# Optimization experiments

Hardware: AMD Instinct MI355X
Metric: run time of the kernel (lower is better)

The kernel has to match this reference:

```python
import jax, jax.numpy as jnp
import numpy as np

NUM_HEADS = 16
FEAT_DIM = 1024
COORD_DIM = 128
D_FEAT = FEAT_DIM // NUM_HEADS   # 64
D_COORD = COORD_DIM // NUM_HEADS # 8

def setup_inputs() -> dict:
    key = jax.random.key(0)
    ks = jax.random.split(key, 5)
    B, L, S = 2, 2048, 2048
    qf = jax.random.normal(ks[0], (B, L, FEAT_DIM), dtype=jnp.float32)
    kf = jax.random.normal(ks[1], (B, S, FEAT_DIM), dtype=jnp.float32)
    qc = jax.random.normal(ks[2], (B, L, COORD_DIM), dtype=jnp.float32)
    kc = jax.random.normal(ks[3], (B, S, COORD_DIM), dtype=jnp.float32)
    v = jax.random.normal(ks[4], (B, S, FEAT_DIM), dtype=jnp.float32)
    alpha = jnp.ones((NUM_HEADS,), dtype=jnp.float32)
    return {"qf": qf, "kf": kf, "qc": qc, "kc": kc, "v": v, "alpha": alpha}

def _split_heads(x):
    # (B, L, H*D) -> (B, H, L, D)
    B, L, HD = x.shape
    return x.reshape(B, L, NUM_HEADS, HD // NUM_HEADS).transpose(0, 2, 1, 3)

def reference(qf, kf, qc, kc, v, alpha):
    qfh = _split_heads(qf)  # (B,H,L,Df)
    kfh = _split_heads(kf)  # (B,H,S,Df)
    qch = _split_heads(qc)  # (B,H,L,Dc)
    kch = _split_heads(kc)  # (B,H,S,Dc)
    vh = _split_heads(v)    # (B,H,S,Dv)
    # A = softmax(Qf Kf^T / sqrt(Df) + alpha * Qc Kc^T / sqrt(Dc))
    inv_sf = 1.0 / np.sqrt(D_FEAT).astype(np.float32)
    inv_sc = 1.0 / np.sqrt(D_COORD).astype(np.float32)
    scores = (jnp.einsum('bhld,bhsd->bhls', qfh, kfh) * inv_sf
              + alpha[None, :, None, None]
              * jnp.einsum('bhld,bhsd->bhls', qch, kch) * inv_sc)
    attn = jax.nn.softmax(scores, axis=-1)
    out = jnp.einsum('bhls,bhsd->bhld', attn, vh)  # (B,H,L,Dv)
    B, H, L, Dv = out.shape
    return out.transpose(0, 2, 1, 3).reshape(B, L, H * Dv)
```

## Files before the change

### kernel.cpp

```cpp
#include <hip/hip_runtime.h>
#include <hip/hip_bf16.h>

typedef __bf16 bf16_t;
typedef bf16_t bf16x8 __attribute__((ext_vector_type(8)));
typedef float f32x4 __attribute__((ext_vector_type(4)));
typedef float f32x16 __attribute__((ext_vector_type(16)));

#define NHEADS 16
#define DFEAT 64
#define DCOORD 8
#define SEQ 2048
#define KVBLK 64
#define NT (SEQ / KVBLK)
#define QBLK 128
#define KCOLS 96
#define KROWB (KCOLS * 2)
#define KTILEB (KVBLK * KROWB)
#define VTILEB (KVBLK * DFEAT * 2)
#define VTILE_ELEMS (KVBLK * DFEAT)

#define KP_BYTES ((size_t)32 * NT * KTILEB)
#define VT_BYTES ((size_t)32 * NT * VTILEB)

union Bf8 { bf16x8 v; __hip_bfloat16 e[8]; };
union U4  { unsigned u[4]; bf16x8 v; };

static __device__ inline unsigned pack2(float a, float b) {
    union { __hip_bfloat16 h[2]; unsigned u; } x;
    x.h[0] = __float2bfloat16(a); x.h[1] = __float2bfloat16(b);
    return x.u;
}

__global__ __launch_bounds__(256)
void pack_k(const float* __restrict__ kf, const float* __restrict__ kc,
            char* __restrict__ kp)
{
    __shared__ __align__(16) char tile[KTILEB];
    const int blk = blockIdx.x;
    const int t  = blk & (NT - 1);
    const int bh = blk >> 5;
    const int b = bh >> 4, h = bh & 15;
    const int tid = threadIdx.x;
    #pragma unroll
    for (int it = 0; it < 2; ++it) {
        const int c = tid + it * 256;
        if (c < 384) {
            const int row = c / 6, cc = c - row * 6;
            const int s = t * KVBLK + row;
            float v[16];
            if (cc < 4) {
                const float* p = kf + ((long)b * SEQ + s) * (NHEADS * DFEAT) + h * DFEAT + cc * 16;
                #pragma unroll
                for (int i = 0; i < 4; ++i) {
                    float4 f = ((const float4*)p)[i];
                    v[4*i+0]=f.x; v[4*i+1]=f.y; v[4*i+2]=f.z; v[4*i+3]=f.w;
                }
            } else if (cc == 4) {
                const float* p = kc + ((long)b * SEQ + s) * (NHEADS * DCOORD) + h * DCOORD;
                float4 f0 = ((const float4*)p)[0];
                float4 f1 = ((const float4*)p)[1];
                v[0]=f0.x; v[1]=f0.y; v[2]=f0.z; v[3]=f0.w;
                v[4]=f1.x; v[5]=f1.y; v[6]=f1.z; v[7]=f1.w;
                #pragma unroll
                for (int i = 8; i < 16; ++i) v[i] = 0.f;
            } else {
                #pragma unroll
                for (int i = 0; i < 16; ++i) v[i] = 0.f;
            }
            Bf8 w0, w1;
            #pragma unroll
            for (int i = 0; i < 8; ++i) {
                w0.e[i] = __float2bfloat16(v[i]);
                w1.e[i] = __float2bfloat16(v[i + 8]);
            }
            const int key  = ((cc < 4) ? (row & 7) : (row & 3)) << 4;
            const int base = cc * 32;
            *(bf16x8*)&tile[row * KROWB + ((base)      ^ key)] = w0.v;
            *(bf16x8*)&tile[row * KROWB + ((base + 16) ^ key)] = w1.v;
        }
    }
    __syncthreads();
    const bf16x8* ti = (const bf16x8*)tile;
    bf16x8* o = (bf16x8*)(kp + (long)blk * KTILEB);
    #pragma unroll
    for (int j = 0; j < 3; ++j) o[tid + 256 * j] = ti[tid + 256 * j];
}

__global__ __launch_bounds__(256)
void pack_v(const float* __restrict__ v, __hip_bfloat16* __restrict__ vt)
{
    __shared__ __align__(16) __hip_bfloat16 tile[VTILE_ELEMS];
    const int blk = blockIdx.x;
    const int t  = blk & (NT - 1);
    const int bh = blk >> 5;
    const int b = bh >> 4, h = bh & 15;
    const int tid = threadIdx.x;
    const int s = tid >> 2, c = tid & 3;
    const int slot = (s & ~12) | ((s & 4) << 1) | ((s & 8) >> 1);
    const float* src = v + ((long)b * SEQ + t * KVBLK + s) * (NHEADS * DFEAT) + h * DFEAT;
    #pragma unroll
    for (int c4 = 0; c4 < 4; ++c4) {
        float4 f = ((const float4*)src)[c4 * 4 + c];
        float vals[4] = {f.x, f.y, f.z, f.w};
        #pragma unroll
        for (int ii = 0; ii < 4; ++ii) {
            const int dd = c4 * 16 + c * 4 + ii;
            const int byte = (dd * 128 + slot * 2) ^ ((dd & 7) << 4);
            tile[byte >> 1] = __float2bfloat16(vals[ii]);
        }
    }
    __syncthreads();
    const bf16x8* ti = (const bf16x8*)tile;
    bf16x8* o = (bf16x8*)(vt + (long)blk * VTILE_ELEMS);
    o[tid]       = ti[tid];
    o[tid + 256] = ti[tid + 256];
}

__global__ __launch_bounds__(256, 2)
void stfa_v5(const float* __restrict__ qf, const float* __restrict__ qc,
             const float* __restrict__ alpha,
             const char* __restrict__ kp, const char* __restrict__ vt,
             float* __restrict__ out)
{
    __shared__ __align__(16) char Kbuf[2][KTILEB];
    __shared__ __align__(16) char Vbuf[2][VTILEB];

    const int tid  = threadIdx.x;
    const int wave = tid >> 6;
    const int lane = tid & 63;
    const int lq   = lane & 31;
    const int hi   = lane >> 5;

    const int dd    = blockIdx.x;
    const int bh    = dd & 31;
    const int qtile = dd >> 5;
    const int b = bh >> 4, h = bh & 15;

    const float a_h      = alpha[h];
    const float LOG2E    = 1.4426950408889634f;
    const float qf_scale = 0.125f * LOG2E;
    const float qc_scale = a_h * 0.35355339059327373f * LOG2E;

    const char* kp_bh = kp + (long)bh * NT * KTILEB;
    const char* vt_bh = (const char*)vt + (long)bh * NT * VTILEB;

    auto stage = [&](int bb, int t) {
        const char* kg = kp_bh + (long)t * KTILEB;
        const char* vg = vt_bh + (long)t * VTILEB;
        char* kl = &Kbuf[bb][0];
        char* vl = &Vbuf[bb][0];
        #pragma unroll
        for (int j = 0; j < 3; ++j) {
            const int i = wave + 4 * j;
            __builtin_amdgcn_global_load_lds(
                (const __attribute__((address_space(1))) void*)(kg + i * 1024 + lane * 16),
                (__attribute__((address_space(3))) void*)(kl + i * 1024), 16, 0, 0);
        }
        #pragma unroll
        for (int j = 0; j < 2; ++j) {
            const int i = wave * 2 + j;
            __builtin_amdgcn_global_load_lds(
                (const __attribute__((address_space(1))) void*)(vg + i * 1024 + lane * 16),
                (__attribute__((address_space(3))) void*)(vl + i * 1024), 16, 0, 0);
        }
    };

    stage(0, 0);

    const int qrow = qtile * QBLK + wave * 32 + lq;
    const float* qfp = qf + ((long)b * SEQ + qrow) * (NHEADS * DFEAT) + h * DFEAT;
    const float* qcp = qc + ((long)b * SEQ + qrow) * (NHEADS * DCOORD) + h * DCOORD;

    bf16x8 qfrag[5];
    #pragma unroll
    for (int ks = 0; ks < 4; ++ks) {
        const float* p = qfp + ks * 16 + hi * 8;
        float4 f0 = *(const float4*)p;
        float4 f1 = *(const float4*)(p + 4);
        Bf8 q;
        q.e[0] = __float2bfloat16(f0.x * qf_scale); q.e[1] = __float2bfloat16(f0.y * qf_scale);
        q.e[2] = __float2bfloat16(f0.z * qf_scale); q.e[3] = __float2bfloat16(f0.w * qf_scale);
        q.e[4] = __float2bfloat16(f1.x * qf_scale); q.e[5] = __float2bfloat16(f1.y * qf_scale);
        q.e[6] = __float2bfloat16(f1.z * qf_scale); q.e[7] = __float2bfloat16(f1.w * qf_scale);
        qfrag[ks] = q.v;
    }
    {
        Bf8 q;
        #pragma unroll
        for (int i = 0; i < 8; ++i) q.e[i] = __float2bfloat16(0.0f);
        if (hi == 0) {
            float4 c0 = *(const float4*)qcp;
            float4 c1 = *(const float4*)(qcp + 4);
            q.e[0] = __float2bfloat16(c0.x * qc_scale); q.e[1] = __float2bfloat16(c0.y * qc_scale);
            q.e[2] = __float2bfloat16(c0.z * qc_scale); q.e[3] = __float2bfloat16(c0.w * qc_scale);
            q.e[4] = __float2bfloat16(c1.x * qc_scale); q.e[5] = __float2bfloat16(c1.y * qc_scale);
            q.e[6] = __float2bfloat16(c1.z * qc_scale); q.e[7] = __float2bfloat16(c1.w * qc_scale);
        }
        qfrag[4] = q.v;
    }

    f32x16 oacc[2];
    #pragma unroll
    for (int dt = 0; dt < 2; ++dt)
        #pragma unroll
        for (int r = 0; r < 16; ++r) oacc[dt][r] = 0.f;
    float l_part = 0.f;

    __syncthreads();

    for (int t = 0; t < NT; ++t) {
        const int bb = t & 1;
        if (t + 1 < NT) stage(bb ^ 1, t + 1);

        f32x16 sacc[2];
        #pragma unroll
        for (int st = 0; st < 2; ++st)
            #pragma unroll
            for (int r = 0; r < 16; ++r) sacc[st][r] = 0.f;
        __builtin_amdgcn_s_setprio(1);
        #pragma unroll
        for (int st = 0; st < 2; ++st) {
            const int row = st * 32 + lq;
            #pragma unroll
            for (int ks = 0; ks < 5; ++ks) {
                const int off = ks * 32 + hi * 16;
                const int key = ((ks < 4) ? (lq & 7) : (lq & 3)) << 4;
                bf16x8 kfrag = *(const bf16x8*)&Kbuf[bb][row * KROWB + (off ^ key)];
                sacc[st] = __builtin_amdgcn_mfma_f32_32x32x16_bf16(kfrag, qfrag[ks], sacc[st], 0, 0, 0);
            }
        }
        __builtin_amdgcn_s_setprio(0);

        bf16x8 pfrag[4];
        float lsum = 0.f;
        #pragma unroll
        for (int T = 0; T < 2; ++T) {
            float p[16];
            #pragma unroll
            for (int r = 0; r < 16; ++r) p[r] = __builtin_amdgcn_exp2f(sacc[T][r]);
            U4 fa, fb;
            #pragma unroll
            for (int i = 0; i < 4; ++i) {
                fa.u[i] = pack2(p[2 * i],     p[2 * i + 1]);
                fb.u[i] = pack2(p[2 * i + 8], p[2 * i + 9]);
            }
            pfrag[2 * T]     = fa.v;
            pfrag[2 * T + 1] = fb.v;
            float s8[8];
            #pragma unroll
            for (int r = 0; r < 8; ++r) s8[r] = p[r] + p[r + 8];
            float s4[4];
            #pragma unroll
            for (int r = 0; r < 4; ++r) s4[r] = s8[r] + s8[r + 4];
            lsum += (s4[0] + s4[1]) + (s4[2] + s4[3]);
        }
        l_part += lsum;

        __builtin_amdgcn_s_setprio(1);
        #pragma unroll
        for (int dt = 0; dt < 2; ++dt) {
            const int row = dt * 32 + lq;
            #pragma unroll
            for (int ks = 0; ks < 4; ++ks) {
                bf16x8 vfrag = *(const bf16x8*)&Vbuf[bb][row * 128 + ((ks * 32 + hi * 16) ^ ((lq & 7) << 4))];
                oacc[dt] = __builtin_amdgcn_mfma_f32_32x32x16_bf16(vfrag, pfrag[ks], oacc[dt], 0, 0, 0);
            }
        }
        __builtin_amdgcn_s_setprio(0);

        __syncthreads();
    }

    const float l = l_part + __shfl_xor(l_part, 32);
    const float invl = 1.0f / l;

    float* ob = out + ((long)b * SEQ + qrow) * (NHEADS * DFEAT) + h * DFEAT;
    #pragma unroll
    for (int dt = 0; dt < 2; ++dt) {
        #pragma unroll
        for (int g = 0; g < 4; ++g) {
            const int d0 = dt * 32 + g * 8 + hi * 4;
            float4 o;
            o.x = oacc[dt][4 * g + 0] * invl;
            o.y = oacc[dt][4 * g + 1] * invl;
            o.z = oacc[dt][4 * g + 2] * invl;
            o.w = oacc[dt][4 * g + 3] * invl;
            *(float4*)(ob + d0) = o;
        }
    }
}

__global__ __launch_bounds__(256)
void stfa_v1(const float* __restrict__ qf, const float* __restrict__ kf,
             const float* __restrict__ qc, const float* __restrict__ kc,
             const float* __restrict__ vv, const float* __restrict__ alpha,
             float* __restrict__ out)
{
    __shared__ __align__(16) __hip_bfloat16 Klds[64 * 104];
    __shared__ __align__(16) __hip_bfloat16 Vlds[64 * 72];
    __shared__ __align__(16) __hip_bfloat16 Plds[4 * 16 * 72];

    const int tid  = threadIdx.x;
    const int wave = tid >> 6;
    const int lane = tid & 63;
    const int lr   = lane & 15;
    const int lg   = lane >> 4;

    const int blk   = blockIdx.x;
    const int qtile = blk & 31;
    const int h     = (blk >> 5) & 15;
    const int b     = blk >> 9;

    for (int i = tid; i < 64 * 104; i += 256) Klds[i] = __float2bfloat16(0.0f);

    const float a_h      = alpha[h];
    const float LOG2E    = 1.4426950408889634f;
    const float qf_scale = 0.125f * LOG2E;
    const float qc_scale = a_h * 0.35355339059327373f * LOG2E;

    const int qrow = qtile * 64 + wave * 16 + lr;
    const float* qf_p = qf + ((long)b * SEQ + qrow) * 1024 + h * 64;
    const float* qc_p = qc + ((long)b * SEQ + qrow) * 128 + h * 8;

    bf16x8 qfrag[3];
    #pragma unroll
    for (int st = 0; st < 2; ++st) {
        const float* p = qf_p + st * 32 + lg * 8;
        float4 f0 = *(const float4*)p;
        float4 f1 = *(const float4*)(p + 4);
        Bf8 q;
        q.e[0] = __float2bfloat16(f0.x * qf_scale); q.e[1] = __float2bfloat16(f0.y * qf_scale);
        q.e[2] = __float2bfloat16(f0.z * qf_scale); q.e[3] = __float2bfloat16(f0.w * qf_scale);
        q.e[4] = __float2bfloat16(f1.x * qf_scale); q.e[5] = __float2bfloat16(f1.y * qf_scale);
        q.e[6] = __float2bfloat16(f1.z * qf_scale); q.e[7] = __float2bfloat16(f1.w * qf_scale);
        qfrag[st] = q.v;
    }
    {
        Bf8 q;
        #pragma unroll
        for (int i = 0; i < 8; ++i) q.e[i] = __float2bfloat16(0.0f);
        if (lg == 0) {
            float4 c0 = *(const float4*)qc_p;
            float4 c1 = *(const float4*)(qc_p + 4);
            q.e[0] = __float2bfloat16(c0.x * qc_scale); q.e[1] = __float2bfloat16(c0.y * qc_scale);
            q.e[2] = __float2bfloat16(c0.z * qc_scale); q.e[3] = __float2bfloat16(c0.w * qc_scale);
            q.e[4] = __float2bfloat16(c1.x * qc_scale); q.e[5] = __float2bfloat16(c1.y * qc_scale);
            q.e[6] = __float2bfloat16(c1.z * qc_scale); q.e[7] = __float2bfloat16(c1.w * qc_scale);
        }
        qfrag[2] = q.v;
    }

    const float* kf_b = kf + (long)b * SEQ * 1024 + h * 64;
    const float* kc_b = kc + (long)b * SEQ * 128 + h * 8;
    const float* v_b  = vv + (long)b * SEQ * 1024 + h * 64;

    f32x4 oacc[4];
    #pragma unroll
    for (int ct = 0; ct < 4; ++ct) { oacc[ct][0]=0.f; oacc[ct][1]=0.f; oacc[ct][2]=0.f; oacc[ct][3]=0.f; }
    float m_r[4], l_r[4];
    #pragma unroll
    for (int j = 0; j < 4; ++j) { m_r[j] = -3.0e38f; l_r[j] = 0.f; }

    __syncthreads();

    for (int s0 = 0; s0 < SEQ; s0 += 64) {
        {
            const int srow = tid >> 2, ch = tid & 3;
            const float* p = kf_b + (long)(s0 + srow) * 1024 + ch * 16;
            float4 f0 = ((const float4*)p)[0];
            float4 f1 = ((const float4*)p)[1];
            float4 f2 = ((const float4*)p)[2];
            float4 f3 = ((const float4*)p)[3];
            Bf8 w0, w1;
            w0.e[0]=__float2bfloat16(f0.x); w0.e[1]=__float2bfloat16(f0.y);
            w0.e[2]=__float2bfloat16(f0.z); w0.e[3]=__float2bfloat16(f0.w);
            w0.e[4]=__float2bfloat16(f1.x); w0.e[5]=__float2bfloat16(f1.y);
            w0.e[6]=__float2bfloat16(f1.z); w0.e[7]=__float2bfloat16(f1.w);
            w1.e[0]=__float2bfloat16(f2.x); w1.e[1]=__float2bfloat16(f2.y);
            w1.e[2]=__float2bfloat16(f2.z); w1.e[3]=__float2bfloat16(f2.w);
            w1.e[4]=__float2bfloat16(f3.x); w1.e[5]=__float2bfloat16(f3.y);
            w1.e[6]=__float2bfloat16(f3.z); w1.e[7]=__float2bfloat16(f3.w);
            *(bf16x8*)&Klds[srow * 104 + ch * 16]     = w0.v;
            *(bf16x8*)&Klds[srow * 104 + ch * 16 + 8] = w1.v;
        }
        {
            const int srow = tid >> 2, cp = (tid & 3) * 2;
            const float* p = kc_b + (long)(s0 + srow) * 128 + cp;
            float2 c = *(const float2*)p;
            Klds[srow * 104 + 64 + cp]     = __float2bfloat16(c.x);
            Klds[srow * 104 + 64 + cp + 1] = __float2bfloat16(c.y);
        }
        {
            const int srow = tid & 63, d0 = (tid >> 6) * 16;
            const float* p = v_b + (long)(s0 + srow) * 1024 + d0;
            #pragma unroll
            for (int c4 = 0; c4 < 4; ++c4) {
                float4 f = ((const float4*)p)[c4];
                Vlds[(d0 + c4 * 4 + 0) * 72 + srow] = __float2bfloat16(f.x);
                Vlds[(d0 + c4 * 4 + 1) * 72 + srow] = __float2bfloat16(f.y);
                Vlds[(d0 + c4 * 4 + 2) * 72 + srow] = __float2bfloat16(f.z);
                Vlds[(d0 + c4 * 4 + 3) * 72 + srow] = __float2bfloat16(f.w);
            }
        }
        __syncthreads();

        f32x4 sacc[4];
        #pragma unroll
        for (int ct = 0; ct < 4; ++ct) { sacc[ct][0]=0.f; sacc[ct][1]=0.f; sacc[ct][2]=0.f; sacc[ct][3]=0.f; }
        #pragma unroll
        for (int ct = 0; ct < 4; ++ct) {
            #pragma unroll
            for (int st = 0; st < 3; ++st) {
                bf16x8 kfrag = *(const bf16x8*)&Klds[(ct * 16 + lr) * 104 + st * 32 + lg * 8];
                sacc[ct] = __builtin_amdgcn_mfma_f32_16x16x32_bf16(qfrag[st], kfrag, sacc[ct], 0, 0, 0);
            }
        }

        float rs[4];
        #pragma unroll
        for (int j = 0; j < 4; ++j) {
            float mx = fmaxf(fmaxf(sacc[0][j], sacc[1][j]), fmaxf(sacc[2][j], sacc[3][j]));
            mx = fmaxf(mx, __shfl_xor(mx, 1));
            mx = fmaxf(mx, __shfl_xor(mx, 2));
            mx = fmaxf(mx, __shfl_xor(mx, 4));
            mx = fmaxf(mx, __shfl_xor(mx, 8));
            float nm = fmaxf(m_r[j], mx);
            rs[j] = __builtin_amdgcn_exp2f(m_r[j] - nm);
            m_r[j] = nm;
        }
        __hip_bfloat16* myP = Plds + wave * 16 * 72;
        #pragma unroll
        for (int j = 0; j < 4; ++j) {
            float p0 = __builtin_amdgcn_exp2f(sacc[0][j] - m_r[j]);
            float p1 = __builtin_amdgcn_exp2f(sacc[1][j] - m_r[j]);
            float p2 = __builtin_amdgcn_exp2f(sacc[2][j] - m_r[j]);
            float p3 = __builtin_amdgcn_exp2f(sacc[3][j] - m_r[j]);
            const int r = lg * 4 + j;
            myP[r * 72 +  0 + lr] = __float2bfloat16(p0);
            myP[r * 72 + 16 + lr] = __float2bfloat16(p1);
            myP[r * 72 + 32 + lr] = __float2bfloat16(p2);
            myP[r * 72 + 48 + lr] = __float2bfloat16(p3);
            float sum = p0 + p1 + p2 + p3;
            sum += __shfl_xor(sum, 1);
            sum += __shfl_xor(sum, 2);
            sum += __shfl_xor(sum, 4);
            sum += __shfl_xor(sum, 8);
            l_r[j] = l_r[j] * rs[j] + sum;
            oacc[0][j] *= rs[j]; oacc[1][j] *= rs[j];
            oacc[2][j] *= rs[j]; oacc[3][j] *= rs[j];
        }

        #pragma unroll
        for (int kk = 0; kk < 2; ++kk) {
            bf16x8 pfrag = *(const bf16x8*)&myP[lr * 72 + kk * 32 + lg * 8];
            #pragma unroll
            for (int ct = 0; ct < 4; ++ct) {
                bf16x8 vfrag = *(const bf16x8*)&Vlds[(ct * 16 + lr) * 72 + kk * 32 + lg * 8];
                oacc[ct] = __builtin_amdgcn_mfma_f32_16x16x32_bf16(pfrag, vfrag, oacc[ct], 0, 0, 0);
            }
        }
        __syncthreads();
    }

    #pragma unroll
    for (int j = 0; j < 4; ++j) {
        const float invl = 1.0f / l_r[j];
        const int q = qtile * 64 + wave * 16 + lg * 4 + j;
        float* op = out + ((long)b * SEQ + q) * 1024 + h * 64;
        op[ 0 + lr] = oacc[0][j] * invl;
        op[16 + lr] = oacc[1][j] * invl;
        op[32 + lr] = oacc[2][j] * invl;
        op[48 + lr] = oacc[3][j] * invl;
    }
}

extern "C" void kernel_launch(void* const* d_in, const int* in_sizes, int n_in,
                              void* d_out, int out_size, void* d_ws, size_t ws_size,
                              hipStream_t stream) {
    const float* qf    = (const float*)d_in[0];
    const float* kf    = (const float*)d_in[1];
    const float* qc    = (const float*)d_in[2];
    const float* kc    = (const float*)d_in[3];
    const float* vv    = (const float*)d_in[4];
    const float* alpha = (const float*)d_in[5];
    float* out = (float*)d_out;

    const int B = 2;
    if (ws_size >= KP_BYTES + VT_BYTES) {
        char* kp = (char*)d_ws;
        __hip_bfloat16* vt = (__hip_bfloat16*)((char*)d_ws + KP_BYTES);
        pack_k<<<B * NHEADS * NT, 256, 0, stream>>>(kf, kc, kp);
        pack_v<<<B * NHEADS * NT, 256, 0, stream>>>(vv, vt);
        stfa_v5<<<B * NHEADS * (SEQ / QBLK), 256, 0, stream>>>(qf, qc, alpha, kp, (const char*)vt, out);
    } else {
        stfa_v1<<<B * NHEADS * (SEQ / 64), 256, 0, stream>>>(qf, kf, qc, kc, vv, alpha, out);
    }
}
```

Baseline: 69.44 us.

## Split KV tile across wave pairs, halve query block, and fuse K/V packing

The attention kernel now uses 64-query blocks, with pairs of waves sharing each 32-query group. Each wave in a pair handles half of every 64-key tile, and the two partial outputs and row sums are merged through shared memory at the end. The change doubles the grid and raises the occupancy target so there is more parallelism across CUs. The K and V packing kernels are fused into one launch, and the V swizzle is changed to match the new half-tile reads. In exchange, each key/value tile is loaded by twice as many blocks and the kernel adds a shared-memory reduction step.

```diff
diff --git a/kernel.cpp b/kernel.cpp
--- a/kernel.cpp
+++ b/kernel.cpp
@@ -12,7 +12,7 @@
 #define SEQ 2048
 #define KVBLK 64
 #define NT (SEQ / KVBLK)
-#define QBLK 128
+#define QBLK 64
 #define KCOLS 96
 #define KROWB (KCOLS * 2)
 #define KTILEB (KVBLK * KROWB)
@@ -32,92 +32,92 @@
 }
 
 __global__ __launch_bounds__(256)
-void pack_k(const float* __restrict__ kf, const float* __restrict__ kc,
-            char* __restrict__ kp)
+void pack_kv(const float* __restrict__ kf, const float* __restrict__ kc,
+             const float* __restrict__ v,
+             char* __restrict__ kp, char* __restrict__ vt)
 {
     __shared__ __align__(16) char tile[KTILEB];
-    const int blk = blockIdx.x;
-    const int t  = blk & (NT - 1);
-    const int bh = blk >> 5;
-    const int b = bh >> 4, h = bh & 15;
+    const int bid = blockIdx.x;
     const int tid = threadIdx.x;
-    #pragma unroll
-    for (int it = 0; it < 2; ++it) {
-        const int c = tid + it * 256;
-        if (c < 384) {
-            const int row = c / 6, cc = c - row * 6;
-            const int s = t * KVBLK + row;
-            float v[16];
-            if (cc < 4) {
-                const float* p = kf + ((long)b * SEQ + s) * (NHEADS * DFEAT) + h * DFEAT + cc * 16;
+
+    if (bid < 1024) {
+        const int blk = bid;
+        const int t  = blk & (NT - 1);
+        const int bh = blk >> 5;
+        const int b = bh >> 4, h = bh & 15;
+        #pragma unroll
+        for (int it = 0; it < 2; ++it) {
+            const int c = tid + it * 256;
+            if (c < 384) {
+                const int row = c / 6, cc = c - row * 6;
+                const int s = t * KVBLK + row;
+                float vv[16];
+                if (cc < 4) {
+                    const float* p = kf + ((long)b * SEQ + s) * (NHEADS * DFEAT) + h * DFEAT + cc * 16;
+                    #pragma unroll
+                    for (int i = 0; i < 4; ++i) {
+                        float4 f = ((const float4*)p)[i];
+                        vv[4*i+0]=f.x; vv[4*i+1]=f.y; vv[4*i+2]=f.z; vv[4*i+3]=f.w;
+                    }
+                } else if (cc == 4) {
+                    const float* p = kc + ((long)b * SEQ + s) * (NHEADS * DCOORD) + h * DCOORD;
+                    float4 f0 = ((const float4*)p)[0];
+                    float4 f1 = ((const float4*)p)[1];
+                    vv[0]=f0.x; vv[1]=f0.y; vv[2]=f0.z; vv[3]=f0.w;
+                    vv[4]=f1.x; vv[5]=f1.y; vv[6]=f1.z; vv[7]=f1.w;
+                    #pragma unroll
+                    for (int i = 8; i < 16; ++i) vv[i] = 0.f;
+                } else {
+                    #pragma unroll
+                    for (int i = 0; i < 16; ++i) vv[i] = 0.f;
+                }
+                Bf8 w0, w1;
                 #pragma unroll
-                for (int i = 0; i < 4; ++i) {
-                    float4 f = ((const float4*)p)[i];
-                    v[4*i+0]=f.x; v[4*i+1]=f.y; v[4*i+2]=f.z; v[4*i+3]=f.w;
+                for (int i = 0; i < 8; ++i) {
+                    w0.e[i] = __float2bfloat16(vv[i]);
+                    w1.e[i] = __float2bfloat16(vv[i + 8]);
                 }
-            } else if (cc == 4) {
-                const float* p = kc + ((long)b * SEQ + s) * (NHEADS * DCOORD) + h * DCOORD;
-                float4 f0 = ((const float4*)p)[0];
-                float4 f1 = ((const float4*)p)[1];
-                v[0]=f0.x; v[1]=f0.y; v[2]=f0.z; v[3]=f0.w;
-                v[4]=f1.x; v[5]=f1.y; v[6]=f1.z; v[7]=f1.w;
-                #pragma unroll
-                for (int i = 8; i < 16; ++i) v[i] = 0.f;
-            } else {
-                #pragma unroll
-                for (int i = 0; i < 16; ++i) v[i] = 0.f;
-            }
-            Bf8 w0, w1;
-            #pragma unroll
-            for (int i = 0; i < 8; ++i) {
-                w0.e[i] = __float2bfloat16(v[i]);
-                w1.e[i] = __float2bfloat16(v[i + 8]);
-            }
-            const int key  = ((cc < 4) ? (row & 7) : (row & 3)) << 4;
-            const int base = cc * 32;
-            *(bf16x8*)&tile[row * KROWB + ((base)      ^ key)] = w0.v;
-            *(bf16x8*)&tile[row * KROWB + ((base + 16) ^ key)] = w1.v;
-        }
-    }
-    __syncthreads();
-    const bf16x8* ti = (const bf16x8*)tile;
-    bf16x8* o = (bf16x8*)(kp + (long)blk * KTILEB);
-    #pragma unroll
-    for (int j = 0; j < 3; ++j) o[tid + 256 * j] = ti[tid + 256 * j];
+                const int key  = ((cc < 4) ? (row & 7) : (row & 3)) << 4;
+                const int base = cc * 32;
+                *(bf16x8*)&tile[row * KROWB + ((base)      ^ key)] = w0.v;
+                *(bf16x8*)&tile[row * KROWB + ((base + 16) ^ key)] = w1.v;
+            }
+        }
+        __syncthreads();
+        const bf16x8* ti = (const bf16x8*)tile;
+        bf16x8* o = (bf16x8*)(kp + (long)blk * KTILEB);
+        #pragma unroll
+        for (int j = 0; j < 3; ++j) o[tid + 256 * j] = ti[tid + 256 * j];
+    } else {
+        const int blk = bid - 1024;
+        const int t  = blk & (NT - 1);
+        const int bh = blk >> 5;
+        const int b = bh >> 4, h = bh & 15;
+        __hip_bfloat16* vtile = (__hip_bfloat16*)tile;
+        const int s = tid >> 2, c = tid & 3;
+        const int slot = (s & ~12) | ((s & 4) << 1) | ((s & 8) >> 1);
+        const float* src = v + ((long)b * SEQ + t * KVBLK + s) * (NHEADS * DFEAT) + h * DFEAT;
+        #pragma unroll
+        for (int c4 = 0; c4 < 4; ++c4) {
+            float4 f = ((const float4*)src)[c4 * 4 + c];
+            float vals[4] = {f.x, f.y, f.z, f.w};
+            #pragma unroll
+            for (int ii = 0; ii < 4; ++ii) {
+                const int dd = c4 * 16 + c * 4 + ii;
+                const int byte = (dd * 128 + slot * 2) ^ ((dd & 3) << 4);
+                vtile[byte >> 1] = __float2bfloat16(vals[ii]);
+            }
+        }
+        __syncthreads();
+        const bf16x8* ti = (const bf16x8*)vtile;
+        bf16x8* o = (bf16x8*)(vt + (long)blk * (long)VTILEB);
+        o[tid]       = ti[tid];
+        o[tid + 256] = ti[tid + 256];
+    }
 }
 
-__global__ __launch_bounds__(256)
-void pack_v(const float* __restrict__ v, __hip_bfloat16* __restrict__ vt)
-{
-    __shared__ __align__(16) __hip_bfloat16 tile[VTILE_ELEMS];
-    const int blk = blockIdx.x;
-    const int t  = blk & (NT - 1);
-    const int bh = blk >> 5;
-    const int b = bh >> 4, h = bh & 15;
-    const int tid = threadIdx.x;
-    const int s = tid >> 2, c = tid & 3;
-    const int slot = (s & ~12) | ((s & 4) << 1) | ((s & 8) >> 1);
-    const float* src = v + ((long)b * SEQ + t * KVBLK + s) * (NHEADS * DFEAT) + h * DFEAT;
-    #pragma unroll
-    for (int c4 = 0; c4 < 4; ++c4) {
-        float4 f = ((const float4*)src)[c4 * 4 + c];
-        float vals[4] = {f.x, f.y, f.z, f.w};
-        #pragma unroll
-        for (int ii = 0; ii < 4; ++ii) {
-            const int dd = c4 * 16 + c * 4 + ii;
-            const int byte = (dd * 128 + slot * 2) ^ ((dd & 7) << 4);
-            tile[byte >> 1] = __float2bfloat16(vals[ii]);
-        }
-    }
-    __syncthreads();
-    const bf16x8* ti = (const bf16x8*)tile;
-    bf16x8* o = (bf16x8*)(vt + (long)blk * VTILE_ELEMS);
-    o[tid]       = ti[tid];
-    o[tid + 256] = ti[tid + 256];
-}
-
-__global__ __launch_bounds__(256, 2)
-void stfa_v5(const float* __restrict__ qf, const float* __restrict__ qc,
+__global__ __launch_bounds__(256, 4)
+void stfa_v6(const float* __restrict__ qf, const float* __restrict__ qc,
              const float* __restrict__ alpha,
              const char* __restrict__ kp, const char* __restrict__ vt,
              float* __restrict__ out)
@@ -130,6 +130,8 @@
     const int lane = tid & 63;
     const int lq   = lane & 31;
     const int hi   = lane >> 5;
+    const int qg   = wave >> 1;
+    const int sh   = wave & 1;
 
     const int dd    = blockIdx.x;
     const int bh    = dd & 31;
@@ -142,7 +144,7 @@
     const float qc_scale = a_h * 0.35355339059327373f * LOG2E;
 
     const char* kp_bh = kp + (long)bh * NT * KTILEB;
-    const char* vt_bh = (const char*)vt + (long)bh * NT * VTILEB;
+    const char* vt_bh = vt + (long)bh * NT * VTILEB;
 
     auto stage = [&](int bb, int t) {
         const char* kg = kp_bh + (long)t * KTILEB;
@@ -167,7 +169,7 @@
 
     stage(0, 0);
 
-    const int qrow = qtile * QBLK + wave * 32 + lq;
+    const int qrow = qtile * QBLK + qg * 32 + lq;
     const float* qfp = qf + ((long)b * SEQ + qrow) * (NHEADS * DFEAT) + h * DFEAT;
     const float* qcp = qc + ((long)b * SEQ + qrow) * (NHEADS * DCOORD) + h * DCOORD;
 
@@ -212,57 +214,52 @@
         const int bb = t & 1;
         if (t + 1 < NT) stage(bb ^ 1, t + 1);
 
-        f32x16 sacc[2];
-        #pragma unroll
-        for (int st = 0; st < 2; ++st)
-            #pragma unroll
-            for (int r = 0; r < 16; ++r) sacc[st][r] = 0.f;
+        f32x16 sacc;
+        #pragma unroll
+        for (int r = 0; r < 16; ++r) sacc[r] = 0.f;
+        const int krow = sh * 32 + lq;
         __builtin_amdgcn_s_setprio(1);
         #pragma unroll
-        for (int st = 0; st < 2; ++st) {
-            const int row = st * 32 + lq;
-            #pragma unroll
-            for (int ks = 0; ks < 5; ++ks) {
-                const int off = ks * 32 + hi * 16;
-                const int key = ((ks < 4) ? (lq & 7) : (lq & 3)) << 4;
-                bf16x8 kfrag = *(const bf16x8*)&Kbuf[bb][row * KROWB + (off ^ key)];
-                sacc[st] = __builtin_amdgcn_mfma_f32_32x32x16_bf16(kfrag, qfrag[ks], sacc[st], 0, 0, 0);
-            }
+        for (int ks = 0; ks < 5; ++ks) {
+            const int off = ks * 32 + hi * 16;
+            const int key = ((ks < 4) ? (lq & 7) : (lq & 3)) << 4;
+            bf16x8 kfrag = *(const bf16x8*)&Kbuf[bb][krow * KROWB + (off ^ key)];
+            sacc = __builtin_amdgcn_mfma_f32_32x32x16_bf16(kfrag, qfrag[ks], sacc, 0, 0, 0);
         }
         __builtin_amdgcn_s_setprio(0);
 
-        bf16x8 pfrag[4];
-        float lsum = 0.f;
-        #pragma unroll
-        for (int T = 0; T < 2; ++T) {
-            float p[16];
-            #pragma unroll
-            for (int r = 0; r < 16; ++r) p[r] = __builtin_amdgcn_exp2f(sacc[T][r]);
+        float p[16];
+        #pragma unroll
+        for (int r = 0; r < 16; ++r) p[r] = __builtin_amdgcn_exp2f(sacc[r]);
+        bf16x8 pfrag[2];
+        {
             U4 fa, fb;
             #pragma unroll
             for (int i = 0; i < 4; ++i) {
                 fa.u[i] = pack2(p[2 * i],     p[2 * i + 1]);
                 fb.u[i] = pack2(p[2 * i + 8], p[2 * i + 9]);
             }
-            pfrag[2 * T]     = fa.v;
-            pfrag[2 * T + 1] = fb.v;
+            pfrag[0] = fa.v;
+            pfrag[1] = fb.v;
+        }
+        {
             float s8[8];
             #pragma unroll
             for (int r = 0; r < 8; ++r) s8[r] = p[r] + p[r + 8];
             float s4[4];
             #pragma unroll
             for (int r = 0; r < 4; ++r) s4[r] = s8[r] + s8[r + 4];
-            lsum += (s4[0] + s4[1]) + (s4[2] + s4[3]);
-        }
-        l_part += lsum;
+            l_part += (s4[0] + s4[1]) + (s4[2] + s4[3]);
+        }
 
         __builtin_amdgcn_s_setprio(1);
         #pragma unroll
         for (int dt = 0; dt < 2; ++dt) {
             const int row = dt * 32 + lq;
             #pragma unroll
-            for (int ks = 0; ks < 4; ++ks) {
-                bf16x8 vfrag = *(const bf16x8*)&Vbuf[bb][row * 128 + ((ks * 32 + hi * 16) ^ ((lq & 7) << 4))];
+            for (int ks = 0; ks < 2; ++ks) {
+                bf16x8 vfrag = *(const bf16x8*)&Vbuf[bb][row * 128 + sh * 64 +
+                                   ((ks * 32 + hi * 16) ^ ((lq & 3) << 4))];
                 oacc[dt] = __builtin_amdgcn_mfma_f32_32x32x16_bf16(vfrag, pfrag[ks], oacc[dt], 0, 0, 0);
             }
         }
@@ -271,21 +268,41 @@
         __syncthreads();
     }
 
-    const float l = l_part + __shfl_xor(l_part, 32);
-    const float invl = 1.0f / l;
-
-    float* ob = out + ((long)b * SEQ + qrow) * (NHEADS * DFEAT) + h * DFEAT;
-    #pragma unroll
-    for (int dt = 0; dt < 2; ++dt) {
-        #pragma unroll
-        for (int g = 0; g < 4; ++g) {
-            const int d0 = dt * 32 + g * 8 + hi * 4;
-            float4 o;
-            o.x = oacc[dt][4 * g + 0] * invl;
-            o.y = oacc[dt][4 * g + 1] * invl;
-            o.z = oacc[dt][4 * g + 2] * invl;
-            o.w = oacc[dt][4 * g + 3] * invl;
-            *(float4*)(ob + d0) = o;
+    float l2 = l_part + __shfl_xor(l_part, 32);
+
+    float* sO = (float*)&Kbuf[0][0];
+    float* sL = (float*)&Vbuf[0][0];
+    if (sh == 1) {
+        float* dst = sO + (qg * 64 + lane) * 32;
+        #pragma unroll
+        for (int dt = 0; dt < 2; ++dt)
+            #pragma unroll
+            for (int r = 0; r < 16; ++r) dst[dt * 16 + r] = oacc[dt][r];
+        sL[qg * 64 + lane] = l2;
+    }
+    __syncthreads();
+    if (sh == 0) {
+        const float* src = sO + (qg * 64 + lane) * 32;
+        #pragma unroll
+        for (int dt = 0; dt < 2; ++dt)
+            #pragma unroll
+            for (int r = 0; r < 16; ++r) oacc[dt][r] += src[dt * 16 + r];
+        const float lT = l2 + sL[qg * 64 + lane];
+        const float invl = 1.0f / lT;
+
+        float* ob = out + ((long)b * SEQ + qrow) * (NHEADS * DFEAT) + h * DFEAT;
+        #pragma unroll
+        for (int dt = 0; dt < 2; ++dt) {
+            #pragma unroll
+            for (int g = 0; g < 4; ++g) {
+                const int d0 = dt * 32 + g * 8 + hi * 4;
+                float4 o;
+                o.x = oacc[dt][4 * g + 0] * invl;
+                o.y = oacc[dt][4 * g + 1] * invl;
+                o.z = oacc[dt][4 * g + 2] * invl;
+                o.w = oacc[dt][4 * g + 3] * invl;
+                *(float4*)(ob + d0) = o;
+            }
         }
     }
 }
@@ -488,10 +505,9 @@
     const int B = 2;
     if (ws_size >= KP_BYTES + VT_BYTES) {
         char* kp = (char*)d_ws;
-        __hip_bfloat16* vt = (__hip_bfloat16*)((char*)d_ws + KP_BYTES);
-        pack_k<<<B * NHEADS * NT, 256, 0, stream>>>(kf, kc, kp);
-        pack_v<<<B * NHEADS * NT, 256, 0, stream>>>(vv, vt);
-        stfa_v5<<<B * NHEADS * (SEQ / QBLK), 256, 0, stream>>>(qf, qc, alpha, kp, (const char*)vt, out);
+        char* vt = (char*)d_ws + KP_BYTES;
+        pack_kv<<<2 * B * NHEADS * NT, 256, 0, stream>>>(kf, kc, vv, kp, vt);
+        stfa_v6<<<B * NHEADS * (SEQ / QBLK), 256, 0, stream>>>(qf, qc, alpha, kp, vt, out);
     } else {
         stfa_v1<<<B * NHEADS * (SEQ / 64), 256, 0, stream>>>(qf, kf, qc, kc, vv, alpha, out);
     }
```

Result: slower. 74.34 us (+7.1%).
